# Performance work log

Hardware: AMD Instinct MI355X
Metric: run time of the kernel (lower is better)

Reference implementation:

```python
import jax, jax.numpy as jnp
import numpy as np

N_EMBD = 1024
N_HEAD = 16
HEAD_SIZE = N_EMBD // N_HEAD
EPS = 1e-5


def layer_norm(x, gamma, beta):
    mu = jnp.mean(x, axis=-1, keepdims=True)
    var = jnp.var(x, axis=-1, keepdims=True)
    return (x - mu) * jax.lax.rsqrt(var + EPS) * gamma + beta


def setup_inputs() -> dict:
    key = jax.random.key(0)
    ks = jax.random.split(key, 12)
    B, T, C, H, hs = 2, 2048, N_EMBD, N_HEAD, HEAD_SIZE
    s = lambda fan_in: 1.0 / np.sqrt(fan_in)
    return {
        "x": jax.random.normal(ks[0], (B, T, C), dtype=jnp.float32),
        "Wq": jax.random.normal(ks[1], (H, C, hs), dtype=jnp.float32) * s(C),
        "Wk": jax.random.normal(ks[2], (H, C, hs), dtype=jnp.float32) * s(C),
        "Wv": jax.random.normal(ks[3], (H, C, hs), dtype=jnp.float32) * s(C),
        "Wproj": jax.random.normal(ks[4], (C, C), dtype=jnp.float32) * s(C),
        "bproj": jax.random.normal(ks[5], (C,), dtype=jnp.float32) * 0.01,
        "g1": jnp.ones((C,), dtype=jnp.float32),
        "b1": jnp.zeros((C,), dtype=jnp.float32),
        "g2": jnp.ones((C,), dtype=jnp.float32),
        "b2": jnp.zeros((C,), dtype=jnp.float32),
        "W_ff1": jax.random.normal(ks[6], (C, 4 * C), dtype=jnp.float32) * s(C),
        "b_ff1": jax.random.normal(ks[7], (4 * C,), dtype=jnp.float32) * 0.01,
        "W_ff2": jax.random.normal(ks[8], (4 * C, C), dtype=jnp.float32) * s(4 * C),
        "b_ff2": jax.random.normal(ks[9], (C,), dtype=jnp.float32) * 0.01,
    }


def reference(x, Wq, Wk, Wv, Wproj, bproj, g1, b1, g2, b2, W_ff1, b_ff1, W_ff2, b_ff2):
    B, T, C = x.shape
    # --- LN1 + multi-head causal self-attention ---
    h = layer_norm(x, g1, b1)
    q = jnp.einsum("btc,hcd->bhtd", h, Wq)  # [B,H,T,hs]
    k = jnp.einsum("btc,hcd->bhtd", h, Wk)
    v = jnp.einsum("btc,hcd->bhtd", h, Wv)
    scale = HEAD_SIZE ** -0.5
    wei = jnp.einsum("bhtd,bhsd->bhts", q, k) * scale  # [B,H,T,T]
    mask = jnp.tril(jnp.ones((T, T), dtype=bool))
    wei = jnp.where(mask, wei, -jnp.inf)
    wei = jax.nn.softmax(wei, axis=-1)
    out = jnp.einsum("bhts,bhsd->bhtd", wei, v)  # [B,H,T,hs]
    out = out.transpose(0, 2, 1, 3).reshape(B, T, C)  # concat heads
    sa = out @ Wproj + bproj
    x = x + sa
    # --- LN2 + FFN ---
    h2 = layer_norm(x, g2, b2)
    ff = jax.nn.relu(h2 @ W_ff1 + b_ff1) @ W_ff2 + b_ff2
    return x + ff
```

## Files before the change

### kernel.cpp

```cpp
#include <hip/hip_runtime.h>
#include <hip/hip_bf16.h>

#define N_EMBD 1024
#define N_HEAD 16
#define HEADSZ 64
#define BATCH  2
#define SEQ    2048
#define ROWS   (BATCH*SEQ)

typedef __attribute__((ext_vector_type(8))) short bf16x8;
typedef __attribute__((ext_vector_type(4))) float f32x4;

__device__ __forceinline__ short f2bs(float v){
    union { __hip_bfloat16 b; short s; } u; u.b = __float2bfloat16(v); return u.s;
}
__device__ __forceinline__ short scale8th(short s){
    union { unsigned i; float f; } u; u.i = ((unsigned)(unsigned short)s) << 16;
    return f2bs(u.f * 0.125f);
}
__device__ __forceinline__ void gload16(const short* g, short* l){
    __builtin_amdgcn_global_load_lds(
        (const __attribute__((address_space(1))) unsigned int*)g,
        (__attribute__((address_space(3))) unsigned int*)l, 16, 0, 0);
}

__global__ __launch_bounds__(256) void tr_cvt(const float* __restrict__ in,
                                              short* __restrict__ out,
                                              int R, int Cc,
                                              size_t in_z, size_t out_z)
{
    __shared__ float t[32][33];
    const int tx = threadIdx.x & 31, ty = threadIdx.x >> 5;
    const int j0 = blockIdx.x * 32, i0 = blockIdx.y * 32;
    const float* ip = in + (size_t)blockIdx.z * in_z;
    short* op = out + (size_t)blockIdx.z * out_z;
#pragma unroll
    for (int p = 0; p < 4; ++p)
        t[ty + p * 8][tx] = ip[(size_t)(i0 + ty + p * 8) * Cc + j0 + tx];
    __syncthreads();
#pragma unroll
    for (int p = 0; p < 4; ++p)
        op[(size_t)(j0 + ty + p * 8) * R + i0 + tx] = f2bs(t[tx][ty + p * 8]);
}

__global__ __launch_bounds__(256) void tr3_cvt(const float* __restrict__ Wq,
                                               const float* __restrict__ Wk,
                                               const float* __restrict__ Wv,
                                               short* __restrict__ w2t)
{
    __shared__ float t[32][33];
    const int tx = threadIdx.x & 31, ty = threadIdx.x >> 5;
    const int which = blockIdx.z >> 4, head = blockIdx.z & 15;
    const int j0 = blockIdx.x * 32, i0 = blockIdx.y * 32;
    const float* ip = (which == 0 ? Wq : which == 1 ? Wk : Wv) + (size_t)head * 65536;
    short* op = w2t + (size_t)which * 1048576 + (size_t)head * 65536;
#pragma unroll
    for (int p = 0; p < 4; ++p)
        t[ty + p * 8][tx] = ip[(size_t)(i0 + ty + p * 8) * 64 + j0 + tx];
    __syncthreads();
#pragma unroll
    for (int p = 0; p < 4; ++p)
        op[(size_t)(j0 + ty + p * 8) * 1024 + i0 + tx] = f2bs(t[tx][ty + p * 8]);
}

__global__ __launch_bounds__(256) void vt_tr(const short* __restrict__ qkv,
                                             short* __restrict__ vt)
{
    __shared__ short t[64][65];
    const int tid = threadIdx.x;
    const int sr = tid >> 2, sc = (tid & 3) * 16;
    const int col0 = blockIdx.x * 64, tok0 = blockIdx.y * 64;
    const short* ip = qkv + (size_t)(tok0 + sr) * 3072 + 2048 + col0 + sc;
    bf16x8 v0 = *(const bf16x8*)ip;
    bf16x8 v1 = *(const bf16x8*)(ip + 8);
#pragma unroll
    for (int i = 0; i < 8; ++i) { t[sr][sc + i] = v0[i]; t[sr][sc + 8 + i] = v1[i]; }
    __syncthreads();
    bf16x8 a, bq;
#pragma unroll
    for (int i = 0; i < 8; ++i) { a[i] = t[sc + i][sr]; bq[i] = t[sc + 8 + i][sr]; }
    short* op = vt + (size_t)(col0 + sr) * 4096 + tok0 + sc;
    *(bf16x8*)op = a;
    *(bf16x8*)(op + 8) = bq;
}

__global__ __launch_bounds__(256) void ln_k(const float* __restrict__ x,
                                            const float* __restrict__ g,
                                            const float* __restrict__ bta,
                                            short* __restrict__ out)
{
    const int row = blockIdx.x;
    const int tid = threadIdx.x;
    const float* xr = x + (size_t)row * N_EMBD;
    float4 v = *(const float4*)(xr + tid * 4);
    float s  = v.x + v.y + v.z + v.w;
    float s2 = v.x * v.x + v.y * v.y + v.z * v.z + v.w * v.w;
#pragma unroll
    for (int off = 32; off; off >>= 1) {
        s  += __shfl_xor(s,  off, 64);
        s2 += __shfl_xor(s2, off, 64);
    }
    __shared__ float rs[4], rs2[4];
    const int wave = tid >> 6, lane = tid & 63;
    if (lane == 0) { rs[wave] = s; rs2[wave] = s2; }
    __syncthreads();
    s  = rs[0] + rs[1] + rs[2] + rs[3];
    s2 = rs2[0] + rs2[1] + rs2[2] + rs2[3];
    const float mean = s * (1.f / N_EMBD);
    const float var  = s2 * (1.f / N_EMBD) - mean * mean;
    const float rsig = rsqrtf(var + 1e-5f);
    float4 gv = *(const float4*)(g + tid * 4);
    float4 bv = *(const float4*)(bta + tid * 4);
    short4 o;
    o.x = f2bs((v.x - mean) * rsig * gv.x + bv.x);
    o.y = f2bs((v.y - mean) * rsig * gv.y + bv.y);
    o.z = f2bs((v.z - mean) * rsig * gv.z + bv.z);
    o.w = f2bs((v.w - mean) * rsig * gv.w + bv.w);
    *(short4*)(out + (size_t)row * N_EMBD + tid * 4) = o;
}

__global__ __launch_bounds__(256) void pln_fin(const float* __restrict__ p0,
                                               const float* __restrict__ p1,
                                               const float* __restrict__ bias,
                                               const float* __restrict__ x,
                                               const float* __restrict__ g,
                                               const float* __restrict__ bta,
                                               float* __restrict__ x2,
                                               short* __restrict__ h2)
{
    const int row = blockIdx.x, tid = threadIdx.x;
    const size_t base = (size_t)row * N_EMBD + tid * 4;
    float4 a  = *(const float4*)(p0 + base);
    float4 c  = *(const float4*)(p1 + base);
    float4 xx = *(const float4*)(x + base);
    float4 bb = *(const float4*)(bias + tid * 4);
    float4 v;
    v.x = a.x + c.x + xx.x + bb.x;
    v.y = a.y + c.y + xx.y + bb.y;
    v.z = a.z + c.z + xx.z + bb.z;
    v.w = a.w + c.w + xx.w + bb.w;
    *(float4*)(x2 + base) = v;
    float s  = v.x + v.y + v.z + v.w;
    float s2 = v.x * v.x + v.y * v.y + v.z * v.z + v.w * v.w;
#pragma unroll
    for (int off = 32; off; off >>= 1) {
        s  += __shfl_xor(s,  off, 64);
        s2 += __shfl_xor(s2, off, 64);
    }
    __shared__ float rs[4], rs2[4];
    const int wave = tid >> 6, lane = tid & 63;
    if (lane == 0) { rs[wave] = s; rs2[wave] = s2; }
    __syncthreads();
    s  = rs[0] + rs[1] + rs[2] + rs[3];
    s2 = rs2[0] + rs2[1] + rs2[2] + rs2[3];
    const float mean = s * (1.f / N_EMBD);
    const float var  = s2 * (1.f / N_EMBD) - mean * mean;
    const float rsig = rsqrtf(var + 1e-5f);
    float4 gv = *(const float4*)(g + tid * 4);
    float4 bv = *(const float4*)(bta + tid * 4);
    short4 o;
    o.x = f2bs((v.x - mean) * rsig * gv.x + bv.x);
    o.y = f2bs((v.y - mean) * rsig * gv.y + bv.y);
    o.z = f2bs((v.z - mean) * rsig * gv.z + bv.z);
    o.w = f2bs((v.w - mean) * rsig * gv.w + bv.w);
    *(short4*)(h2 + base) = o;
}

__global__ __launch_bounds__(256) void mfma_gemm(
    const short* __restrict__ A,
    const short* __restrict__ Bt,
    const float* __restrict__ bias,
    const float* __restrict__ resid,
    float* __restrict__ outf,
    float* __restrict__ outf2,
    short* __restrict__ outb,
    int M, int N, int K, int kz, int relu)
{
    __shared__ __align__(16) short As[128 * 32];
    __shared__ __align__(16) short Bs[128 * 32];
    const int tid  = threadIdx.x;
    const int lane = tid & 63, w = tid >> 6;
    const int quad = lane >> 4, l16 = lane & 15;
    const int row0 = blockIdx.y * 128, col0 = blockIdx.x * 128;
    const int wm = (w >> 1) * 64, wn = (w & 1) * 64;
    const int koff = blockIdx.z * kz;
    const int kend = kz ? kz : K;

    f32x4 acc[4][4];
#pragma unroll
    for (int i = 0; i < 4; ++i)
#pragma unroll
        for (int j = 0; j < 4; ++j)
            acc[i][j] = f32x4{0.f, 0.f, 0.f, 0.f};

    const int c0  = w * 128 + lane;
    const int c1  = c0 + 64;
    const int ar0 = c0 >> 2, ak0 = (((c0 & 3) ^ ((ar0 >> 1) & 3))) * 8;
    const int ar1 = c1 >> 2, ak1 = (((c1 & 3) ^ ((ar1 >> 1) & 3))) * 8;
    const short* aG0 = A  + (size_t)(row0 + ar0) * K + koff + ak0;
    const short* aG1 = A  + (size_t)(row0 + ar1) * K + koff + ak1;
    const short* bG0 = Bt + (size_t)(col0 + ar0) * K + koff + ak0;
    const short* bG1 = Bt + (size_t)(col0 + ar1) * K + koff + ak1;
    short* aL0 = As + (size_t)w * 1024;
    short* aL1 = aL0 + 512;
    short* bL0 = Bs + (size_t)w * 1024;
    short* bL1 = bL0 + 512;

    const int gsw = (quad ^ ((l16 >> 1) & 3)) * 8;

    for (int k0 = 0; k0 < kend; k0 += 32) {
        __syncthreads();
        gload16(aG0 + k0, aL0);
        gload16(aG1 + k0, aL1);
        gload16(bG0 + k0, bL0);
        gload16(bG1 + k0, bL1);
        asm volatile("s_waitcnt vmcnt(0)" ::: "memory");
        __syncthreads();

        bf16x8 af[4], bfr[4];
#pragma unroll
        for (int i = 0; i < 4; ++i)
            af[i]  = *(const bf16x8*)(As + (wm + i * 16 + l16) * 32 + gsw);
#pragma unroll
        for (int j = 0; j < 4; ++j)
            bfr[j] = *(const bf16x8*)(Bs + (wn + j * 16 + l16) * 32 + gsw);
#pragma unroll
        for (int i = 0; i < 4; ++i)
#pragma unroll
            for (int j = 0; j < 4; ++j)
                acc[i][j] = __builtin_amdgcn_mfma_f32_16x16x32_bf16(
                    af[i], bfr[j], acc[i][j], 0, 0, 0);
    }

    float* of = blockIdx.z ? outf2 : outf;
#pragma unroll
    for (int i = 0; i < 4; ++i) {
        const int rbase = row0 + wm + i * 16 + quad * 4;
#pragma unroll
        for (int j = 0; j < 4; ++j) {
            const int c = col0 + wn + j * 16 + l16;
            const float bv = bias ? bias[c] : 0.f;
#pragma unroll
            for (int r = 0; r < 4; ++r) {
                float v = acc[i][j][r] + bv;
                if (relu) v = fmaxf(v, 0.f);
                const size_t idx = (size_t)(rbase + r) * N + c;
                if (resid) v += resid[idx];
                if (outb) outb[idx] = f2bs(v);
                else      of[idx] = v;
            }
        }
    }
}

__global__ __launch_bounds__(256) void ff2_fin(const float* __restrict__ p0,
                                               const float* __restrict__ bias,
                                               const float* __restrict__ x2,
                                               float* __restrict__ out)
{
    const size_t i = ((size_t)blockIdx.x * 256 + threadIdx.x) * 4;
    float4 a = *(const float4*)(p0 + i);
    float4 b = *(const float4*)(out + i);
    float4 r = *(const float4*)(x2 + i);
    float4 bb = *(const float4*)(bias + (i & 1023));
    float4 o;
    o.x = a.x + b.x + r.x + bb.x;
    o.y = a.y + b.y + r.y + bb.y;
    o.z = a.z + b.z + r.z + bb.z;
    o.w = a.w + b.w + r.w + bb.w;
    *(float4*)(out + i) = o;
}

__global__ __launch_bounds__(256) void attn_k(const short* __restrict__ qkv,
                                              const short* __restrict__ vt,
                                              short* __restrict__ att)
{
    __shared__ __align__(16) short Ks[2][64 * 64];
    __shared__ __align__(16) short Vs[2][64 * 64];
    __shared__ __align__(16) short Ps[64 * 72];
    const int tid  = threadIdx.x;
    const int lane = tid & 63, w = tid >> 6;
    const int quad = lane >> 4, l16 = lane & 15;
    const int bh = blockIdx.y, b = bh >> 4, head = bh & 15;

    const int srow = lane >> 3;
    const int sw   = ((lane & 7) ^ srow) * 8;
    const int cidx = (quad ^ (l16 & 7)) * 8;

#pragma unroll
    for (int pass = 0; pass < 2; ++pass) {
        const int qt = pass == 0 ? (int)blockIdx.x : 31 - (int)blockIdx.x;
        const int t0 = qt * 64;
        const int ntiles = qt + 1;

        const short* qp = qkv + (size_t)(b * SEQ + t0 + w * 16 + l16) * 3072
                          + head * 64 + quad * 8;
        bf16x8 qf0 = *(const bf16x8*)qp;
        bf16x8 qf1 = *(const bf16x8*)(qp + 32);
#pragma unroll
        for (int i = 0; i < 8; ++i) { qf0[i] = scale8th(qf0[i]); qf1[i] = scale8th(qf1[i]); }

        float mrow[4], lrow[4];
        f32x4 O[4];
#pragma unroll
        for (int r = 0; r < 4; ++r) { mrow[r] = -INFINITY; lrow[r] = 0.f; }
#pragma unroll
        for (int jn = 0; jn < 4; ++jn) O[jn] = f32x4{0.f, 0.f, 0.f, 0.f};

        asm volatile("s_waitcnt vmcnt(0) lgkmcnt(0)\n\ts_barrier" ::: "memory");
        {
            const short* kg = qkv + (size_t)(b * SEQ + w * 16 + srow) * 3072
                              + 1024 + head * 64 + sw;
            const short* vg = vt + (size_t)(head * 64 + w * 16 + srow) * 4096
                              + b * SEQ + sw;
            short* kL = Ks[0] + w * 1024;
            short* vL = Vs[0] + w * 1024;
            gload16(kg, kL); gload16(kg + (size_t)8 * 3072, kL + 512);
            gload16(vg, vL); gload16(vg + (size_t)8 * 4096, vL + 512);
        }

        for (int kt = 0; kt < ntiles; ++kt) {
            const int cur = kt & 1;
            asm volatile("s_waitcnt vmcnt(0) lgkmcnt(0)\n\ts_barrier" ::: "memory");
            if (kt + 1 < ntiles) {
                const int s1 = (kt + 1) * 64;
                const short* kg = qkv + (size_t)(b * SEQ + s1 + w * 16 + srow) * 3072
                                  + 1024 + head * 64 + sw;
                const short* vg = vt + (size_t)(head * 64 + w * 16 + srow) * 4096
                                  + b * SEQ + s1 + sw;
                short* kL = Ks[cur ^ 1] + w * 1024;
                short* vL = Vs[cur ^ 1] + w * 1024;
                gload16(kg, kL); gload16(kg + (size_t)8 * 3072, kL + 512);
                gload16(vg, vL); gload16(vg + (size_t)8 * 4096, vL + 512);
            }

            f32x4 S[4];
            const short* Kb = Ks[cur];
#pragma unroll
            for (int jn = 0; jn < 4; ++jn) {
                S[jn] = f32x4{0.f, 0.f, 0.f, 0.f};
                const short* kp = Kb + (jn * 16 + l16) * 64;
                bf16x8 b0 = *(const bf16x8*)(kp + cidx);
                bf16x8 b1 = *(const bf16x8*)(kp + (cidx ^ 32));
                S[jn] = __builtin_amdgcn_mfma_f32_16x16x32_bf16(qf0, b0, S[jn], 0, 0, 0);
                S[jn] = __builtin_amdgcn_mfma_f32_16x16x32_bf16(qf1, b1, S[jn], 0, 0, 0);
            }

            float Sv[4][4];
            const int tq = t0 + w * 16 + quad * 4;
            const int s0 = kt * 64;
#pragma unroll
            for (int jn = 0; jn < 4; ++jn)
#pragma unroll
                for (int r = 0; r < 4; ++r)
                    Sv[jn][r] = S[jn][r];
            if (kt == ntiles - 1) {
#pragma unroll
                for (int jn = 0; jn < 4; ++jn)
#pragma unroll
                    for (int r = 0; r < 4; ++r)
                        if (s0 + jn * 16 + l16 > tq + r) Sv[jn][r] = -INFINITY;
            }
#pragma unroll
            for (int r = 0; r < 4; ++r) {
                float rm = fmaxf(fmaxf(Sv[0][r], Sv[1][r]), fmaxf(Sv[2][r], Sv[3][r]));
#pragma unroll
                for (int off = 8; off; off >>= 1) rm = fmaxf(rm, __shfl_xor(rm, off, 64));
                const float mn    = fmaxf(mrow[r], rm);
                const float alpha = __expf(mrow[r] - mn);
                float ps = 0.f;
#pragma unroll
                for (int jn = 0; jn < 4; ++jn) {
                    Sv[jn][r] = __expf(Sv[jn][r] - mn);
                    ps += Sv[jn][r];
                }
#pragma unroll
                for (int off = 8; off; off >>= 1) ps += __shfl_xor(ps, off, 64);
                lrow[r] = lrow[r] * alpha + ps;
                mrow[r] = mn;
#pragma unroll
                for (int jn = 0; jn < 4; ++jn) O[jn][r] *= alpha;
            }

#pragma unroll
            for (int jn = 0; jn < 4; ++jn)
#pragma unroll
                for (int r = 0; r < 4; ++r)
                    Ps[(w * 16 + quad * 4 + r) * 72 + jn * 16 + l16] = f2bs(Sv[jn][r]);
            asm volatile("s_waitcnt lgkmcnt(0)" ::: "memory");

            const short* pp = Ps + (w * 16 + l16) * 72 + quad * 8;
            bf16x8 pf0 = *(const bf16x8*)pp;
            bf16x8 pf1 = *(const bf16x8*)(pp + 32);
            const short* Vb = Vs[cur];
#pragma unroll
            for (int jn = 0; jn < 4; ++jn) {
                const short* vp = Vb + (jn * 16 + l16) * 64;
                bf16x8 v0 = *(const bf16x8*)(vp + cidx);
                bf16x8 v1 = *(const bf16x8*)(vp + (cidx ^ 32));
                O[jn] = __builtin_amdgcn_mfma_f32_16x16x32_bf16(pf0, v0, O[jn], 0, 0, 0);
                O[jn] = __builtin_amdgcn_mfma_f32_16x16x32_bf16(pf1, v1, O[jn], 0, 0, 0);
            }
        }

#pragma unroll
        for (int r = 0; r < 4; ++r) {
            const float inv = 1.f / lrow[r];
            const size_t rowoff = (size_t)(b * SEQ + t0 + w * 16 + quad * 4 + r) * N_EMBD
                                  + head * 64 + l16;
#pragma unroll
            for (int jn = 0; jn < 4; ++jn)
                att[rowoff + jn * 16] = f2bs(O[jn][r] * inv);
        }
    }
}

extern "C" void kernel_launch(void* const* d_in, const int* in_sizes, int n_in,
                              void* d_out, int out_size, void* d_ws, size_t ws_size,
                              hipStream_t stream)
{
    const float* x     = (const float*)d_in[0];
    const float* Wq    = (const float*)d_in[1];
    const float* Wk    = (const float*)d_in[2];
    const float* Wv    = (const float*)d_in[3];
    const float* Wproj = (const float*)d_in[4];
    const float* bproj = (const float*)d_in[5];
    const float* g1    = (const float*)d_in[6];
    const float* b1    = (const float*)d_in[7];
    const float* g2    = (const float*)d_in[8];
    const float* b2    = (const float*)d_in[9];
    const float* Wff1  = (const float*)d_in[10];
    const float* bff1  = (const float*)d_in[11];
    const float* Wff2  = (const float*)d_in[12];
    const float* bff2  = (const float*)d_in[13];
    float* out = (float*)d_out;

    char* ws = (char*)d_ws;
    short* w2t  = (short*)(ws + 0);
    short* wpt  = (short*)(ws + 6291456);
    short* wf1t = (short*)(ws + 8388608);
    short* wf2t = (short*)(ws + 16777216);
    short* h    = (short*)(ws + 25165824);
    short* qkv  = (short*)(ws + 33554432);
    short* vt   = (short*)(ws + 58720256);
    short* att  = (short*)(ws + 67108864);
    float* x2   = (float*)(ws + 75497472);
    short* h2   = h;
    float* p0p  = (float*)(ws + 33554432);
    float* p1p  = (float*)(ws + 50331648);
    short* ff   = qkv;
    float* p0f  = (float*)(ws + 0);

    tr3_cvt<<<dim3(2, 32, 48),  256, 0, stream>>>(Wq, Wk, Wv, w2t);
    tr_cvt<<<dim3(32, 32, 1),  256, 0, stream>>>(Wproj, wpt,  1024, 1024, 0, 0);
    tr_cvt<<<dim3(128, 32, 1), 256, 0, stream>>>(Wff1, wf1t,  1024, 4096, 0, 0);
    tr_cvt<<<dim3(32, 128, 1), 256, 0, stream>>>(Wff2, wf2t,  4096, 1024, 0, 0);

    ln_k<<<ROWS, 256, 0, stream>>>(x, g1, b1, h);
    mfma_gemm<<<dim3(3072 / 128, ROWS / 128), 256, 0, stream>>>(
        h, w2t, nullptr, nullptr, nullptr, nullptr, qkv, ROWS, 3072, N_EMBD, 0, 0);
    vt_tr<<<dim3(16, 64), 256, 0, stream>>>(qkv, vt);
    attn_k<<<dim3(16, BATCH * N_HEAD), 256, 0, stream>>>(qkv, vt, att);
    mfma_gemm<<<dim3(N_EMBD / 128, ROWS / 128, 2), 256, 0, stream>>>(
        att, wpt, nullptr, nullptr, p0p, p1p, nullptr, ROWS, N_EMBD, N_EMBD, 512, 0);
    pln_fin<<<ROWS, 256, 0, stream>>>(p0p, p1p, bproj, x, g2, b2, x2, h2);
    mfma_gemm<<<dim3(4096 / 128, ROWS / 128), 256, 0, stream>>>(
        h2, wf1t, bff1, nullptr, nullptr, nullptr, ff, ROWS, 4096, N_EMBD, 0, 1);
    mfma_gemm<<<dim3(N_EMBD / 128, ROWS / 128, 2), 256, 0, stream>>>(
        ff, wf2t, nullptr, nullptr, p0f, out, nullptr, ROWS, N_EMBD, 4096, 2048, 0);
    ff2_fin<<<ROWS * N_EMBD / 1024, 256, 0, stream>>>(p0f, bff2, x2, out);
}
```

Measured before the change: 421.2 us.

## Deepen GEMM K-tile to 64 and process two query tiles per attention block

```diff
diff --git a/kernel.cpp b/kernel.cpp
--- a/kernel.cpp
+++ b/kernel.cpp
@@ -176,8 +176,8 @@
     short* __restrict__ outb,
     int M, int N, int K, int kz, int relu)
 {
-    __shared__ __align__(16) short As[128 * 32];
-    __shared__ __align__(16) short Bs[128 * 32];
+    __shared__ __align__(16) short As[128 * 64];
+    __shared__ __align__(16) short Bs[128 * 64];
     const int tid  = threadIdx.x;
     const int lane = tid & 63, w = tid >> 6;
     const int quad = lane >> 4, l16 = lane & 15;
@@ -193,43 +193,46 @@
         for (int j = 0; j < 4; ++j)
             acc[i][j] = f32x4{0.f, 0.f, 0.f, 0.f};
 
-    const int c0  = w * 128 + lane;
-    const int c1  = c0 + 64;
-    const int ar0 = c0 >> 2, ak0 = (((c0 & 3) ^ ((ar0 >> 1) & 3))) * 8;
-    const int ar1 = c1 >> 2, ak1 = (((c1 & 3) ^ ((ar1 >> 1) & 3))) * 8;
-    const short* aG0 = A  + (size_t)(row0 + ar0) * K + koff + ak0;
-    const short* aG1 = A  + (size_t)(row0 + ar1) * K + koff + ak1;
-    const short* bG0 = Bt + (size_t)(col0 + ar0) * K + koff + ak0;
-    const short* bG1 = Bt + (size_t)(col0 + ar1) * K + koff + ak1;
-    short* aL0 = As + (size_t)w * 1024;
-    short* aL1 = aL0 + 512;
-    short* bL0 = Bs + (size_t)w * 1024;
-    short* bL1 = bL0 + 512;
-
-    const int gsw = (quad ^ ((l16 >> 1) & 3)) * 8;
-
-    for (int k0 = 0; k0 < kend; k0 += 32) {
+    const short* aG[4]; const short* bG[4];
+#pragma unroll
+    for (int q = 0; q < 4; ++q) {
+        const int L = w * 256 + q * 64 + lane;
+        const int r = L >> 3, c = (L & 7) ^ (r & 7);
+        aG[q] = A  + (size_t)(row0 + r) * K + koff + c * 8;
+        bG[q] = Bt + (size_t)(col0 + r) * K + koff + c * 8;
+    }
+    short* aL = As + w * 2048;
+    short* bL = Bs + w * 2048;
+
+    const int fsw = (quad ^ (l16 & 7)) * 8;
+
+    for (int k0 = 0; k0 < kend; k0 += 64) {
         __syncthreads();
-        gload16(aG0 + k0, aL0);
-        gload16(aG1 + k0, aL1);
-        gload16(bG0 + k0, bL0);
-        gload16(bG1 + k0, bL1);
+#pragma unroll
+        for (int q = 0; q < 4; ++q) {
+            gload16(aG[q] + k0, aL + q * 512);
+            gload16(bG[q] + k0, bL + q * 512);
+        }
         asm volatile("s_waitcnt vmcnt(0)" ::: "memory");
         __syncthreads();
 
-        bf16x8 af[4], bfr[4];
-#pragma unroll
-        for (int i = 0; i < 4; ++i)
-            af[i]  = *(const bf16x8*)(As + (wm + i * 16 + l16) * 32 + gsw);
-#pragma unroll
-        for (int j = 0; j < 4; ++j)
-            bfr[j] = *(const bf16x8*)(Bs + (wn + j * 16 + l16) * 32 + gsw);
-#pragma unroll
-        for (int i = 0; i < 4; ++i)
+#pragma unroll
+        for (int kb = 0; kb < 2; ++kb) {
+            const int fp = fsw ^ (kb * 32);
+            bf16x8 af[4], bfr[4];
+#pragma unroll
+            for (int i = 0; i < 4; ++i)
+                af[i]  = *(const bf16x8*)(As + (wm + i * 16 + l16) * 64 + fp);
 #pragma unroll
             for (int j = 0; j < 4; ++j)
-                acc[i][j] = __builtin_amdgcn_mfma_f32_16x16x32_bf16(
-                    af[i], bfr[j], acc[i][j], 0, 0, 0);
+                bfr[j] = *(const bf16x8*)(Bs + (wn + j * 16 + l16) * 64 + fp);
+#pragma unroll
+            for (int i = 0; i < 4; ++i)
+#pragma unroll
+                for (int j = 0; j < 4; ++j)
+                    acc[i][j] = __builtin_amdgcn_mfma_f32_16x16x32_bf16(
+                        af[i], bfr[j], acc[i][j], 0, 0, 0);
+        }
     }
 
     float* of = blockIdx.z ? outf2 : outf;
@@ -277,7 +280,7 @@
 {
     __shared__ __align__(16) short Ks[2][64 * 64];
     __shared__ __align__(16) short Vs[2][64 * 64];
-    __shared__ __align__(16) short Ps[64 * 72];
+    __shared__ __align__(16) short Ps[128 * 72];
     const int tid  = threadIdx.x;
     const int lane = tid & 63, w = tid >> 6;
     const int quad = lane >> 4, l16 = lane & 15;
@@ -287,74 +290,91 @@
     const int sw   = ((lane & 7) ^ srow) * 8;
     const int cidx = (quad ^ (l16 & 7)) * 8;
 
-#pragma unroll
-    for (int pass = 0; pass < 2; ++pass) {
-        const int qt = pass == 0 ? (int)blockIdx.x : 31 - (int)blockIdx.x;
-        const int t0 = qt * 64;
-        const int ntiles = qt + 1;
-
-        const short* qp = qkv + (size_t)(b * SEQ + t0 + w * 16 + l16) * 3072
+    const int qt = 15 - (int)blockIdx.x;
+    const int q0 = qt * 128;
+    const int ntiles = 2 * qt + 2;
+
+    bf16x8 qf[2][2];
+#pragma unroll
+    for (int s = 0; s < 2; ++s) {
+        const short* qp = qkv + (size_t)(b * SEQ + q0 + s * 64 + w * 16 + l16) * 3072
                           + head * 64 + quad * 8;
-        bf16x8 qf0 = *(const bf16x8*)qp;
-        bf16x8 qf1 = *(const bf16x8*)(qp + 32);
-#pragma unroll
-        for (int i = 0; i < 8; ++i) { qf0[i] = scale8th(qf0[i]); qf1[i] = scale8th(qf1[i]); }
-
-        float mrow[4], lrow[4];
-        f32x4 O[4];
-#pragma unroll
-        for (int r = 0; r < 4; ++r) { mrow[r] = -INFINITY; lrow[r] = 0.f; }
-#pragma unroll
-        for (int jn = 0; jn < 4; ++jn) O[jn] = f32x4{0.f, 0.f, 0.f, 0.f};
-
+        qf[s][0] = *(const bf16x8*)qp;
+        qf[s][1] = *(const bf16x8*)(qp + 32);
+#pragma unroll
+        for (int i = 0; i < 8; ++i) {
+            qf[s][0][i] = scale8th(qf[s][0][i]);
+            qf[s][1][i] = scale8th(qf[s][1][i]);
+        }
+    }
+
+    float mrow[2][4], lrow[2][4];
+    f32x4 O[2][4];
+#pragma unroll
+    for (int s = 0; s < 2; ++s)
+#pragma unroll
+        for (int r = 0; r < 4; ++r) {
+            mrow[s][r] = -INFINITY; lrow[s][r] = 0.f;
+            O[s][r] = f32x4{0.f, 0.f, 0.f, 0.f};
+        }
+
+    {
+        const short* kg = qkv + (size_t)(b * SEQ + w * 16 + srow) * 3072
+                          + 1024 + head * 64 + sw;
+        const short* vg = vt + (size_t)(head * 64 + w * 16 + srow) * 4096
+                          + b * SEQ + sw;
+        short* kL = Ks[0] + w * 1024;
+        short* vL = Vs[0] + w * 1024;
+        gload16(kg, kL); gload16(kg + (size_t)8 * 3072, kL + 512);
+        gload16(vg, vL); gload16(vg + (size_t)8 * 4096, vL + 512);
+    }
+
+    for (int kt = 0; kt < ntiles; ++kt) {
+        const int cur = kt & 1;
         asm volatile("s_waitcnt vmcnt(0) lgkmcnt(0)\n\ts_barrier" ::: "memory");
-        {
-            const short* kg = qkv + (size_t)(b * SEQ + w * 16 + srow) * 3072
+        if (kt + 1 < ntiles) {
+            const int s1 = (kt + 1) * 64;
+            const short* kg = qkv + (size_t)(b * SEQ + s1 + w * 16 + srow) * 3072
                               + 1024 + head * 64 + sw;
             const short* vg = vt + (size_t)(head * 64 + w * 16 + srow) * 4096
-                              + b * SEQ + sw;
-            short* kL = Ks[0] + w * 1024;
-            short* vL = Vs[0] + w * 1024;
+                              + b * SEQ + s1 + sw;
+            short* kL = Ks[cur ^ 1] + w * 1024;
+            short* vL = Vs[cur ^ 1] + w * 1024;
             gload16(kg, kL); gload16(kg + (size_t)8 * 3072, kL + 512);
             gload16(vg, vL); gload16(vg + (size_t)8 * 4096, vL + 512);
         }
 
-        for (int kt = 0; kt < ntiles; ++kt) {
-            const int cur = kt & 1;
-            asm volatile("s_waitcnt vmcnt(0) lgkmcnt(0)\n\ts_barrier" ::: "memory");
-            if (kt + 1 < ntiles) {
-                const int s1 = (kt + 1) * 64;
-                const short* kg = qkv + (size_t)(b * SEQ + s1 + w * 16 + srow) * 3072
-                                  + 1024 + head * 64 + sw;
-                const short* vg = vt + (size_t)(head * 64 + w * 16 + srow) * 4096
-                                  + b * SEQ + s1 + sw;
-                short* kL = Ks[cur ^ 1] + w * 1024;
-                short* vL = Vs[cur ^ 1] + w * 1024;
-                gload16(kg, kL); gload16(kg + (size_t)8 * 3072, kL + 512);
-                gload16(vg, vL); gload16(vg + (size_t)8 * 4096, vL + 512);
+        const bool do0 = (kt <= 2 * qt);
+
+        f32x4 S[2][4];
+        const short* Kb = Ks[cur];
+#pragma unroll
+        for (int jn = 0; jn < 4; ++jn) {
+            const short* kp = Kb + (jn * 16 + l16) * 64;
+            bf16x8 b0 = *(const bf16x8*)(kp + cidx);
+            bf16x8 b1 = *(const bf16x8*)(kp + (cidx ^ 32));
+            if (do0) {
+                S[0][jn] = f32x4{0.f, 0.f, 0.f, 0.f};
+                S[0][jn] = __builtin_amdgcn_mfma_f32_16x16x32_bf16(qf[0][0], b0, S[0][jn], 0, 0, 0);
+                S[0][jn] = __builtin_amdgcn_mfma_f32_16x16x32_bf16(qf[0][1], b1, S[0][jn], 0, 0, 0);
             }
-
-            f32x4 S[4];
-            const short* Kb = Ks[cur];
-#pragma unroll
-            for (int jn = 0; jn < 4; ++jn) {
-                S[jn] = f32x4{0.f, 0.f, 0.f, 0.f};
-                const short* kp = Kb + (jn * 16 + l16) * 64;
-                bf16x8 b0 = *(const bf16x8*)(kp + cidx);
-                bf16x8 b1 = *(const bf16x8*)(kp + (cidx ^ 32));
-                S[jn] = __builtin_amdgcn_mfma_f32_16x16x32_bf16(qf0, b0, S[jn], 0, 0, 0);
-                S[jn] = __builtin_amdgcn_mfma_f32_16x16x32_bf16(qf1, b1, S[jn], 0, 0, 0);
-            }
-
+            S[1][jn] = f32x4{0.f, 0.f, 0.f, 0.f};
+            S[1][jn] = __builtin_amdgcn_mfma_f32_16x16x32_bf16(qf[1][0], b0, S[1][jn], 0, 0, 0);
+            S[1][jn] = __builtin_amdgcn_mfma_f32_16x16x32_bf16(qf[1][1], b1, S[1][jn], 0, 0, 0);
+        }
+
+        const int s0 = kt * 64;
+#pragma unroll
+        for (int s = 0; s < 2; ++s) {
+            if (s == 0 && !do0) continue;
             float Sv[4][4];
-            const int tq = t0 + w * 16 + quad * 4;
-            const int s0 = kt * 64;
+            const int tq = q0 + s * 64 + w * 16 + quad * 4;
 #pragma unroll
             for (int jn = 0; jn < 4; ++jn)
 #pragma unroll
                 for (int r = 0; r < 4; ++r)
-                    Sv[jn][r] = S[jn][r];
-            if (kt == ntiles - 1) {
+                    Sv[jn][r] = S[s][jn][r];
+            if (kt == 2 * qt + s) {
 #pragma unroll
                 for (int jn = 0; jn < 4; ++jn)
 #pragma unroll
@@ -366,8 +386,8 @@
                 float rm = fmaxf(fmaxf(Sv[0][r], Sv[1][r]), fmaxf(Sv[2][r], Sv[3][r]));
 #pragma unroll
                 for (int off = 8; off; off >>= 1) rm = fmaxf(rm, __shfl_xor(rm, off, 64));
-                const float mn    = fmaxf(mrow[r], rm);
-                const float alpha = __expf(mrow[r] - mn);
+                const float mn    = fmaxf(mrow[s][r], rm);
+                const float alpha = __expf(mrow[s][r] - mn);
                 float ps = 0.f;
 #pragma unroll
                 for (int jn = 0; jn < 4; ++jn) {
@@ -376,43 +396,52 @@
                 }
 #pragma unroll
                 for (int off = 8; off; off >>= 1) ps += __shfl_xor(ps, off, 64);
-                lrow[r] = lrow[r] * alpha + ps;
-                mrow[r] = mn;
-#pragma unroll
-                for (int jn = 0; jn < 4; ++jn) O[jn][r] *= alpha;
+                lrow[s][r] = lrow[s][r] * alpha + ps;
+                mrow[s][r] = mn;
+#pragma unroll
+                for (int jn = 0; jn < 4; ++jn) O[s][jn][r] *= alpha;
             }
-
 #pragma unroll
             for (int jn = 0; jn < 4; ++jn)
 #pragma unroll
                 for (int r = 0; r < 4; ++r)
-                    Ps[(w * 16 + quad * 4 + r) * 72 + jn * 16 + l16] = f2bs(Sv[jn][r]);
-            asm volatile("s_waitcnt lgkmcnt(0)" ::: "memory");
-
-            const short* pp = Ps + (w * 16 + l16) * 72 + quad * 8;
-            bf16x8 pf0 = *(const bf16x8*)pp;
-            bf16x8 pf1 = *(const bf16x8*)(pp + 32);
-            const short* Vb = Vs[cur];
-#pragma unroll
-            for (int jn = 0; jn < 4; ++jn) {
-                const short* vp = Vb + (jn * 16 + l16) * 64;
-                bf16x8 v0 = *(const bf16x8*)(vp + cidx);
-                bf16x8 v1 = *(const bf16x8*)(vp + (cidx ^ 32));
-                O[jn] = __builtin_amdgcn_mfma_f32_16x16x32_bf16(pf0, v0, O[jn], 0, 0, 0);
-                O[jn] = __builtin_amdgcn_mfma_f32_16x16x32_bf16(pf1, v1, O[jn], 0, 0, 0);
+                    Ps[(s * 64 + w * 16 + quad * 4 + r) * 72 + jn * 16 + l16] = f2bs(Sv[jn][r]);
+        }
+        asm volatile("s_waitcnt lgkmcnt(0)" ::: "memory");
+
+        bf16x8 pf[2][2];
+#pragma unroll
+        for (int s = 0; s < 2; ++s) {
+            const short* pp = Ps + (s * 64 + w * 16 + l16) * 72 + quad * 8;
+            pf[s][0] = *(const bf16x8*)pp;
+            pf[s][1] = *(const bf16x8*)(pp + 32);
+        }
+        const short* Vb = Vs[cur];
+#pragma unroll
+        for (int jn = 0; jn < 4; ++jn) {
+            const short* vp = Vb + (jn * 16 + l16) * 64;
+            bf16x8 v0 = *(const bf16x8*)(vp + cidx);
+            bf16x8 v1 = *(const bf16x8*)(vp + (cidx ^ 32));
+            if (do0) {
+                O[0][jn] = __builtin_amdgcn_mfma_f32_16x16x32_bf16(pf[0][0], v0, O[0][jn], 0, 0, 0);
+                O[0][jn] = __builtin_amdgcn_mfma_f32_16x16x32_bf16(pf[0][1], v1, O[0][jn], 0, 0, 0);
             }
-        }
-
+            O[1][jn] = __builtin_amdgcn_mfma_f32_16x16x32_bf16(pf[1][0], v0, O[1][jn], 0, 0, 0);
+            O[1][jn] = __builtin_amdgcn_mfma_f32_16x16x32_bf16(pf[1][1], v1, O[1][jn], 0, 0, 0);
+        }
+    }
+
+#pragma unroll
+    for (int s = 0; s < 2; ++s)
 #pragma unroll
         for (int r = 0; r < 4; ++r) {
-            const float inv = 1.f / lrow[r];
-            const size_t rowoff = (size_t)(b * SEQ + t0 + w * 16 + quad * 4 + r) * N_EMBD
-                                  + head * 64 + l16;
+            const float inv = 1.f / lrow[s][r];
+            const size_t rowoff = (size_t)(b * SEQ + q0 + s * 64 + w * 16 + quad * 4 + r)
+                                  * N_EMBD + head * 64 + l16;
 #pragma unroll
             for (int jn = 0; jn < 4; ++jn)
-                att[rowoff + jn * 16] = f2bs(O[jn][r] * inv);
-        }
-    }
+                att[rowoff + jn * 16] = f2bs(O[s][jn][r] * inv);
+        }
 }
 
 extern "C" void kernel_launch(void* const* d_in, const int* in_sizes, int n_in,
```

Result: slower. 434.8 us (+3.2%).
